# Kernel tuning notes

Measured on AMD Instinct MI355X. Metric: run time of the kernel, lower is better.

## Reference

```python
import jax, jax.numpy as jnp
import numpy as np

B, N, D = 8, 1024, 512
H, F = 8, 2048
Dh = D // H
EPS = 1e-5
NEG = -1.0e9


def _layernorm(x, g, b):
    mu = jnp.mean(x, axis=-1, keepdims=True)
    var = jnp.mean(jnp.square(x - mu), axis=-1, keepdims=True)
    return (x - mu) * jax.lax.rsqrt(var + EPS) * g + b


def setup_inputs() -> dict:
    key = jax.random.key(0)
    ks = jax.random.split(key, 8)
    s = 0.02  # weight init scale
    return {
        "x": jax.random.normal(ks[0], (B, N, D), jnp.float32),
        "adjacency_logits": jax.random.normal(ks[1], (N, N), jnp.float32),
        "candidate_edge_mask": jax.random.randint(ks[2], (N, N), 0, 2).astype(jnp.bool_),
        "Wq": jax.random.normal(ks[3], (D, D), jnp.float32) * s,
        "Wk": jax.random.normal(ks[4], (D, D), jnp.float32) * s,
        "Wv": jax.random.normal(ks[5], (D, D), jnp.float32) * s,
        "Wo": jax.random.normal(ks[6], (D, D), jnp.float32) * s,
        "W1": jax.random.normal(jax.random.fold_in(key, 10), (F, D), jnp.float32) * s,
        "b1": jnp.zeros((F,), jnp.float32),
        "W2": jax.random.normal(jax.random.fold_in(key, 11), (D, F), jnp.float32) * s,
        "b2": jnp.zeros((D,), jnp.float32),
        "g_ln1": jnp.ones((D,), jnp.float32),
        "beta_ln1": jnp.zeros((D,), jnp.float32),
        "g_ln2": jnp.ones((D,), jnp.float32),
        "beta_ln2": jnp.zeros((D,), jnp.float32),
    }


def reference(x, adjacency_logits, candidate_edge_mask, Wq, Wk, Wv, Wo,
              W1, b1, W2, b2, g_ln1, beta_ln1, g_ln2, beta_ln2):
    b, n, d = x.shape
    # projections: torch Linear is x @ W^T  -> [B,H,N,Dh]
    def proj(W):
        return jnp.einsum('bnd,ed->bne', x, W).reshape(b, n, H, Dh).transpose(0, 2, 1, 3)
    q, k, v = proj(Wq), proj(Wk), proj(Wv)
    scale = 1.0 / jnp.sqrt(jnp.float32(Dh))
    scores = jnp.einsum('bhqd,bhkd->bhqk', q, k) * scale
    scores = scores + adjacency_logits[None, None]
    mask = candidate_edge_mask[None, None]  # [1,1,N,N]
    scores = jnp.where(mask, scores, NEG)
    attn = jax.nn.softmax(scores, axis=-1)
    attn = jnp.where(mask, attn, 0.0)
    ctx = jnp.einsum('bhqk,bhkd->bhqd', attn, v)
    ctx = ctx.transpose(0, 2, 1, 3).reshape(b, n, d)
    attn_out = jnp.einsum('bnd,ed->bne', ctx, Wo)
    z = _layernorm(x + attn_out, g_ln1, beta_ln1)
    h = jax.nn.relu(jnp.einsum('bnd,fd->bnf', z, W1) + b1)
    z_ffn = jnp.einsum('bnf,df->bnd', h, W2) + b2
    out = _layernorm(z + z_ffn, g_ln2, beta_ln2)
    return out, attn.mean(axis=1)
```

## Files before the change

kernel.cpp:

```cpp
#include <hip/hip_runtime.h>
#include <math.h>
#include <stdint.h>


using bf16_t = __bf16;
typedef __attribute__((__ext_vector_type__(8))) __bf16 bf16x8;
typedef __attribute__((__ext_vector_type__(4))) __bf16 bf16x4;
typedef __attribute__((__ext_vector_type__(4))) float  f32x4;

#define DEVI __device__ __forceinline__

DEVI f32x4 mfma16(bf16x8 a, bf16x8 b, f32x4 c) {
  return __builtin_amdgcn_mfma_f32_16x16x32_bf16(a, b, c, 0, 0, 0);
}

DEVI void gload_lds16(const void* g, void* l) {
  __builtin_amdgcn_global_load_lds(
      (const __attribute__((address_space(1))) uint32_t*)g,
      (__attribute__((address_space(3))) uint32_t*)l, 16, 0, 0);
}

#define EPSC  (1e-5f)
#define QSCALE 0.18033688f

__global__ __launch_bounds__(256) void k_cvtall(const float* __restrict__ x,
                                                const float* __restrict__ wq,
                                                const float* __restrict__ wk,
                                                const float* __restrict__ wv,
                                                const float* __restrict__ wo,
                                                const float* __restrict__ w1,
                                                const float* __restrict__ w2,
                                                const float* __restrict__ adj,
                                                const int* __restrict__ msk,
                                                bf16_t* __restrict__ ox,
                                                bf16_t* __restrict__ owq,
                                                bf16_t* __restrict__ owk,
                                                bf16_t* __restrict__ owv,
                                                bf16_t* __restrict__ owo,
                                                bf16_t* __restrict__ ow1,
                                                bf16_t* __restrict__ ow2,
                                                bf16_t* __restrict__ eadjT) {
  int blk = blockIdx.x;
  if (blk >= 7168) {
    int row  = (blk - 7168) * 4 + (threadIdx.x >> 6);
    int lane = threadIdx.x & 63;
    for (int i = 0; i < 16; i++) {
      int c = lane + 64 * i;
      size_t idx = (size_t)row * 1024 + c;
      float a = adj[idx];
      bool valid = (msk[idx] != 0);
      int pos = (c & ~63) + (((c >> 2) & 3) << 4) + (((c >> 4) & 3) << 2) + (c & 3);
      eadjT[(size_t)row * 1024 + pos] = valid ? (__bf16)__expf(a) : (__bf16)0.f;
    }
    return;
  }
  const float* src; bf16_t* dst; int base;
  if (blk < 4096)      { src = x;  dst = ox;  base = blk; }
  else {
    blk -= 4096;
    if      (blk < 256)  { src = wq; dst = owq; base = blk; }
    else if (blk < 512)  { src = wk; dst = owk; base = blk - 256; }
    else if (blk < 768)  { src = wv; dst = owv; base = blk - 512; }
    else if (blk < 1024) { src = wo; dst = owo; base = blk - 768; }
    else if (blk < 2048) { src = w1; dst = ow1; base = blk - 1024; }
    else                 { src = w2; dst = ow2; base = blk - 2048; }
  }
  int i = base * 256 + threadIdx.x;
  float4 v = ((const float4*)src)[i];
  bf16x4 o = { (__bf16)v.x, (__bf16)v.y, (__bf16)v.z, (__bf16)v.w };
  ((bf16x4*)dst)[i] = o;
}

template<int EPI, int NSPLIT>
__global__ __launch_bounds__(256) void k_gemm(const bf16_t* __restrict__ A,
                                              const bf16_t* __restrict__ B,
                                              int K, int nbx,
                                              const float* __restrict__ bias,
                                              bf16_t* __restrict__ outb,
                                              int out_ncols) {
  __shared__ bf16_t lA[2][4096];
  __shared__ bf16_t lB[2][4096];
  int bid = blockIdx.x;
  int bps = 64 * nbx;
  int split = bid / bps, r = bid - split * bps;
  int nb = r % nbx, mb = r / nbx;
  int KS = K / NSPLIT;
  const bf16_t* Ab = A + (size_t)split * KS;
  const bf16_t* Bb = B + (size_t)split * KS;
  int tid = threadIdx.x, wid = tid >> 6, lane = tid & 63;
  int l16 = lane & 15, g = lane >> 4;
  int wr = wid >> 1, wc = wid & 1;
  int rowbase = mb * 128, c0 = nb * 128;

  int dA0 = wid * 2048 + lane * 16;
  int rA0 = dA0 >> 6;
  int cbA = ((dA0 >> 4) & 3) ^ (rA0 & 3);
  const bf16_t* Asrc0 = Ab + (size_t)(rowbase + rA0) * K + cbA * 8;
  const bf16_t* Asrc1 = Ab + (size_t)(rowbase + rA0 + 16) * K + cbA * 8;
  const bf16_t* Bsrc0 = Bb + (size_t)(c0 + rA0) * K + cbA * 8;
  const bf16_t* Bsrc1 = Bb + (size_t)(c0 + rA0 + 16) * K + cbA * 8;

  f32x4 acc[4][4];
#pragma unroll
  for (int m = 0; m < 4; m++)
#pragma unroll
    for (int n = 0; n < 4; n++) acc[m][n] = (f32x4){0.f, 0.f, 0.f, 0.f};

  gload_lds16(Asrc0, (char*)&lA[0][0] + wid * 2048);
  gload_lds16(Asrc1, (char*)&lA[0][0] + wid * 2048 + 1024);
  gload_lds16(Bsrc0, (char*)&lB[0][0] + wid * 2048);
  gload_lds16(Bsrc1, (char*)&lB[0][0] + wid * 2048 + 1024);
  __syncthreads();

  for (int k0 = 0; k0 < KS; k0 += 32) {
    int buf = (k0 >> 5) & 1;
    if (k0 + 32 < KS) {
      gload_lds16(Asrc0 + k0 + 32, (char*)&lA[buf ^ 1][0] + wid * 2048);
      gload_lds16(Asrc1 + k0 + 32, (char*)&lA[buf ^ 1][0] + wid * 2048 + 1024);
      gload_lds16(Bsrc0 + k0 + 32, (char*)&lB[buf ^ 1][0] + wid * 2048);
      gload_lds16(Bsrc1 + k0 + 32, (char*)&lB[buf ^ 1][0] + wid * 2048 + 1024);
    }
    const char* cA = (const char*)&lA[buf][0];
    const char* cB = (const char*)&lB[buf][0];
    bf16x8 af[4], bq[4];
#pragma unroll
    for (int m = 0; m < 4; m++) {
      int row = wr * 64 + m * 16 + l16;
      af[m] = *(const bf16x8*)(cA + row * 64 + ((g ^ (row & 3)) << 4));
    }
#pragma unroll
    for (int n = 0; n < 4; n++) {
      int row = wc * 64 + n * 16 + l16;
      bq[n] = *(const bf16x8*)(cB + row * 64 + ((g ^ (row & 3)) << 4));
    }
#pragma unroll
    for (int m = 0; m < 4; m++)
#pragma unroll
      for (int n = 0; n < 4; n++) acc[m][n] = mfma16(af[m], bq[n], acc[m][n]);
    __syncthreads();
  }

  int which = c0 / out_ncols;
  int cloc0 = c0 - which * out_ncols;
  size_t obase = (size_t)which * 8192 * out_ncols +
                 (size_t)split * 8192 * out_ncols * (NSPLIT > 1 ? 1 : 0);
  float osc = (EPI == 0 && which == 0) ? QSCALE : 1.0f;
#pragma unroll
  for (int n = 0; n < 4; n++) {
    int col = cloc0 + wc * 64 + n * 16 + l16;
    float bv = (EPI >= 1 && bias && split == 0) ? bias[col] : 0.f;
#pragma unroll
    for (int m = 0; m < 4; m++)
#pragma unroll
      for (int j = 0; j < 4; j++) {
        int row = rowbase + wr * 64 + m * 16 + g * 4 + j;
        float v = acc[m][n][j] + bv;
        size_t idx = obase + (size_t)row * out_ncols + col;
        if (EPI == 1) outb[idx] = (__bf16)fmaxf(v, 0.f);
        else if (EPI == 0) outb[idx] = (__bf16)(v * osc);
        else outb[idx] = (__bf16)v;
      }
  }
}

__global__ __launch_bounds__(256) void k_resln(const bf16_t* __restrict__ gin,
                                               int nsplit,
                                               const float* __restrict__ residf,
                                               const bf16_t* __restrict__ residb,
                                               const float* __restrict__ gam,
                                               const float* __restrict__ bet,
                                               float* __restrict__ outf,
                                               bf16_t* __restrict__ outb) {
  const size_t GS = (size_t)8192 * 512;
  int row = blockIdx.x * 4 + (threadIdx.x >> 6);
  int lane = threadIdx.x & 63;
  const bf16_t* gp = gin + (size_t)row * 512;
  float a[8];
  {
    bf16x8 v = ((const bf16x8*)gp)[lane];
#pragma unroll
    for (int e = 0; e < 8; e++) a[e] = (float)v[e];
  }
  for (int s = 1; s < nsplit; s++) {
    bf16x8 v = ((const bf16x8*)(gp + s * GS))[lane];
#pragma unroll
    for (int e = 0; e < 8; e++) a[e] += (float)v[e];
  }
  if (residf) {
    const float* rp = residf + (size_t)row * 512;
    float4 r0 = ((const float4*)rp)[2 * lane];
    float4 r1 = ((const float4*)rp)[2 * lane + 1];
    a[0] += r0.x; a[1] += r0.y; a[2] += r0.z; a[3] += r0.w;
    a[4] += r1.x; a[5] += r1.y; a[6] += r1.z; a[7] += r1.w;
  } else {
    bf16x8 r = ((const bf16x8*)(residb + (size_t)row * 512))[lane];
#pragma unroll
    for (int e = 0; e < 8; e++) a[e] += (float)r[e];
  }
  float s = 0.f;
#pragma unroll
  for (int e = 0; e < 8; e++) s += a[e];
  for (int off = 1; off < 64; off <<= 1) s += __shfl_xor(s, off);
  float mu = s * (1.f / 512.f);
  float sq = 0.f;
#pragma unroll
  for (int e = 0; e < 8; e++) { float d = a[e] - mu; sq += d * d; }
  for (int off = 1; off < 64; off <<= 1) sq += __shfl_xor(sq, off);
  float rs = rsqrtf(sq * (1.f / 512.f) + EPSC);

  float4 g0 = ((const float4*)gam)[2 * lane], g1v = ((const float4*)gam)[2 * lane + 1];
  float4 b0 = ((const float4*)bet)[2 * lane], b1v = ((const float4*)bet)[2 * lane + 1];
  float o[8];
  o[0] = (a[0] - mu) * rs * g0.x + b0.x;  o[1] = (a[1] - mu) * rs * g0.y + b0.y;
  o[2] = (a[2] - mu) * rs * g0.z + b0.z;  o[3] = (a[3] - mu) * rs * g0.w + b0.w;
  o[4] = (a[4] - mu) * rs * g1v.x + b1v.x; o[5] = (a[5] - mu) * rs * g1v.y + b1v.y;
  o[6] = (a[6] - mu) * rs * g1v.z + b1v.z; o[7] = (a[7] - mu) * rs * g1v.w + b1v.w;
  if (outf) {
    float* op = outf + (size_t)row * 512;
    ((float4*)op)[2 * lane]     = (float4){o[0], o[1], o[2], o[3]};
    ((float4*)op)[2 * lane + 1] = (float4){o[4], o[5], o[6], o[7]};
  }
  if (outb) {
    bf16x8 q;
#pragma unroll
    for (int e = 0; e < 8; e++) q[e] = (__bf16)o[e];
    ((bf16x8*)(outb + (size_t)row * 512))[lane] = q;
  }
}

__global__ __launch_bounds__(256) void k_vtrans_knorm(const bf16_t* __restrict__ v,
                                                      bf16_t* __restrict__ vT,
                                                      const bf16_t* __restrict__ kk,
                                                      float* __restrict__ kmax) {
  __shared__ bf16_t t[64 * 66];
  __shared__ float red[4];
  int bid = blockIdx.x;
  int tid = threadIdx.x, wid = tid >> 6, lane = tid & 63;
  if (bid < 1024) {
    int nt = bid & 15, h = (bid >> 4) & 7, b = bid >> 7;
    for (int i = 0; i < 16; i++) {
      int n = wid * 16 + i;
      t[lane * 66 + n] = v[(size_t)(b * 1024 + nt * 64 + n) * 512 + h * 64 + lane];
    }
    __syncthreads();
    int pi = (lane & 32) + (((lane >> 2) & 3) << 3) + (((lane >> 4) & 1) << 2) + (lane & 3);
    for (int i = 0; i < 16; i++) {
      int d = wid * 16 + i;
      vT[(size_t)((b * 8 + h) * 64 + d) * 1024 + nt * 64 + pi] = t[d * 66 + lane];
    }
  } else {
    int bh = bid - 1024;
    int b = bh >> 3, h = bh & 7;
    float mx = 0.f;
    for (int n = tid; n < 1024; n += 256) {
      const bf16_t* kp = kk + (size_t)(b * 1024 + n) * 512 + h * 64;
      float ss = 0.f;
#pragma unroll
      for (int vv = 0; vv < 8; vv++) {
        bf16x8 kv = *(const bf16x8*)(kp + vv * 8);
#pragma unroll
        for (int e = 0; e < 8; e++) { float f = (float)kv[e]; ss += f * f; }
      }
      mx = fmaxf(mx, ss);
    }
    for (int off = 1; off < 64; off <<= 1) mx = fmaxf(mx, __shfl_xor(mx, off));
    if (lane == 0) red[wid] = mx;
    __syncthreads();
    if (tid == 0) kmax[bh] = sqrtf(fmaxf(fmaxf(red[0], red[1]), fmaxf(red[2], red[3])));
  }
}

__global__ __launch_bounds__(512) void k_attn_ctx(const bf16_t* __restrict__ q,
                                                  const bf16_t* __restrict__ kk,
                                                  const bf16_t* __restrict__ vT,
                                                  const bf16_t* __restrict__ eadjT,
                                                  const float* __restrict__ kmax,
                                                  bf16_t* __restrict__ ctx,
                                                  float* __restrict__ crl) {
  __shared__ bf16_t ldsK[2][4096];
  __shared__ bf16_t ldsV[2][4096];
  int bid = blockIdx.x;
  int qt = bid >> 6, h = bid & 7, b = (bid >> 3) & 7;
  int tid = threadIdx.x, wid = tid >> 6, lane = tid & 63;
  int l16 = lane & 15, g = lane >> 4;
  int qg0 = qt * 128 + wid * 16;
  int kvbase = (b * 8 + h) * 64;

  int d0 = wid * 1024 + lane * 16;
  int row0 = d0 >> 7;
  int cb0 = ((d0 >> 4) & 7) ^ (row0 & 7);
  const bf16_t* ksrc = kk + (size_t)(b * 1024) * 512 + h * 64;
  const bf16_t* vsrc = vT + (size_t)kvbase * 1024;

  auto stage = [&](int buf, int kc0) {
    gload_lds16(ksrc + (size_t)(kc0 + row0) * 512 + cb0 * 8, &ldsK[buf][wid * 512]);
    gload_lds16(vsrc + (size_t)row0 * 1024 + kc0 + cb0 * 8, &ldsV[buf][wid * 512]);
  };

  const bf16_t* qp = q + (size_t)(b * 1024 + qg0 + l16) * 512 + h * 64 + 8 * g;
  bf16x8 aq0 = *(const bf16x8*)qp;
  bf16x8 aq1 = *(const bf16x8*)(qp + 32);

  float kmaxv = kmax[b * 8 + h];
  float ssq = 0.f;
#pragma unroll
  for (int e = 0; e < 8; e++) {
    float f0 = (float)aq0[e], f1 = (float)aq1[e];
    ssq += f0 * f0 + f1 * f1;
  }
  ssq += __shfl_xor(ssq, 16);
  ssq += __shfl_xor(ssq, 32);
  float Cn = sqrtf(ssq) * kmaxv;
  f32x4 negC4 = (f32x4){-Cn, -Cn, -Cn, -Cn};
  float Cj[4];
#pragma unroll
  for (int j = 0; j < 4; j++) Cj[j] = __shfl(Cn, g * 4 + j);

  bf16x8 ones;
#pragma unroll
  for (int e = 0; e < 8; e++) ones[e] = (__bf16)1.0f;

  f32x4 cacc[4];
#pragma unroll
  for (int d = 0; d < 4; d++) cacc[d] = (f32x4){0.f, 0.f, 0.f, 0.f};
  f32x4 lsacc = (f32x4){0.f, 0.f, 0.f, 0.f};
  int rph = l16 & 7;
  const bf16_t* erowT = eadjT + (size_t)(qg0 + l16) * 1024 + g * 16;

  bf16x8 eaA[2], eaB[2];
  auto loadEA = [&](bf16x8 (&d)[2], int kc0) {
    d[0] = *(const bf16x8*)(erowT + kc0);
    d[1] = *(const bf16x8*)(erowT + kc0 + 8);
  };

  auto cbar = [&]() {
    __builtin_amdgcn_sched_barrier(0);
    asm volatile("s_waitcnt vmcnt(2) lgkmcnt(0)" ::: "memory");
    __builtin_amdgcn_sched_barrier(0);
    __builtin_amdgcn_s_barrier();
    __builtin_amdgcn_sched_barrier(0);
  };

  auto tile = [&](int kt, int buf, bf16x8 (&eaC)[2], bf16x8 (&eaN)[2]) {
    int ktn = (kt + 1 < 16) ? kt + 1 : 15;
    stage(buf ^ 1, ktn * 64);
    loadEA(eaN, ktn * 64);

    const char* curK = (const char*)ldsK[buf];
    const char* curV = (const char*)ldsV[buf];

    bf16x8 pa0, pa1;
#pragma unroll
    for (int cg = 0; cg < 4; cg++) {
      const char* krow = curK + ((cg * 16 + l16) << 7);
      bf16x8 k0 = *(const bf16x8*)(krow + ((g ^ rph) << 4));
      bf16x8 k1 = *(const bf16x8*)(krow + (((g + 4) ^ rph) << 4));
      __builtin_amdgcn_s_setprio(1);
      f32x4 s = mfma16(k0, aq0, negC4);
      s = mfma16(k1, aq1, s);
      __builtin_amdgcn_s_setprio(0);
#pragma unroll
      for (int j = 0; j < 4; j++) {
        float p = (float)eaC[cg >> 1][(cg & 1) * 4 + j] * exp2f(s[j]);
        if (cg < 2) pa0[cg * 4 + j] = (__bf16)p;
        else        pa1[(cg - 2) * 4 + j] = (__bf16)p;
      }
    }
#pragma unroll
    for (int half = 0; half < 2; half++) {
      bf16x8 pa = half ? pa1 : pa0;
      __builtin_amdgcn_s_setprio(1);
#pragma unroll
      for (int dg = 0; dg < 4; dg++) {
        const char* vrow = curV + ((dg * 16 + l16) << 7);
        bf16x8 vv = *(const bf16x8*)(vrow + (((g + half * 4) ^ rph) << 4));
        cacc[dg] = mfma16(pa, vv, cacc[dg]);
      }
      lsacc = mfma16(pa, ones, lsacc);
      __builtin_amdgcn_s_setprio(0);
    }
    cbar();
  };

  stage(0, 0);
  loadEA(eaA, 0);
  cbar();

  for (int k2 = 0; k2 < 8; k2++) {
    tile(2 * k2,     0, eaA, eaB);
    tile(2 * k2 + 1, 1, eaB, eaA);
  }

  float rcj[4];
#pragma unroll
  for (int j = 0; j < 4; j++) rcj[j] = (lsacc[j] > 0.f) ? (1.f / lsacc[j]) : 0.f;

#pragma unroll
  for (int dg = 0; dg < 4; dg++)
#pragma unroll
    for (int j = 0; j < 4; j++) {
      int row = qg0 + g * 4 + j;
      ctx[(size_t)(b * 1024 + row) * 512 + h * 64 + dg * 16 + l16] =
          (__bf16)(cacc[dg][j] * rcj[j]);
    }
  if (l16 == 0) {
#pragma unroll
    for (int j = 0; j < 4; j++) {
      int li = (b * 8 + h) * 1024 + qg0 + g * 4 + j;
      crl[li] = (lsacc[j] > 0.f) ? (Cj[j] + __log2f(lsacc[j])) : 1.0e30f;
    }
  }
}

__global__ __launch_bounds__(256, 4) void k_attn_mean(const bf16_t* __restrict__ q,
                                                      const bf16_t* __restrict__ kk,
                                                      const bf16_t* __restrict__ eadjT,
                                                      const float* __restrict__ crl,
                                                      float* __restrict__ mout) {
  __shared__ bf16_t lds[4][2][2048];
  int bid = blockIdx.x;
  int kq = bid & 7, qt = (bid >> 3) & 15, b = bid >> 7;
  int tid = threadIdx.x, wid = tid >> 6, lane = tid & 63;
  int l16 = lane & 15, g = lane >> 4;
  int qg0 = qt * 64 + wid * 16;
  int kbase = kq * 128;
  int rl = lane >> 3;
  int cb = (lane & 7) ^ rl;
  const bf16_t* ksrc = kk + (size_t)(b * 1024 + kbase) * 512;

  auto stage = [&](int t) {
    int h = t >> 2, c = t & 3;
    char* dst = (char*)&lds[wid][t & 1][0];
    const bf16_t* sp = ksrc + (size_t)(c * 32 + rl) * 512 + h * 64 + cb * 8;
#pragma unroll
    for (int i = 0; i < 4; i++)
      gload_lds16(sp + (size_t)i * 8 * 512, dst + i * 1024);
  };

  f32x4 macc[8];
#pragma unroll
  for (int kg = 0; kg < 8; kg++) macc[kg] = (f32x4){0.f, 0.f, 0.f, 0.f};

  stage(0);

  for (int h = 0; h < 8; h++) {
    const bf16_t* qp = q + (size_t)(b * 1024 + qg0 + l16) * 512 + h * 64 + 8 * g;
    bf16x8 aq0 = *(const bf16x8*)qp;
    bf16x8 aq1 = *(const bf16x8*)(qp + 32);
    float CRs = crl[(b * 8 + h) * 1024 + qg0 + l16];
    f32x4 negCR4 = (f32x4){-CRs, -CRs, -CRs, -CRs};
#pragma unroll
    for (int c = 0; c < 4; c++) {
      int t = h * 4 + c;
      __builtin_amdgcn_sched_barrier(0);
      if (t < 31) {
        stage(t + 1);
        __builtin_amdgcn_sched_barrier(0);
        asm volatile("s_waitcnt vmcnt(4)" ::: "memory");
      } else {
        asm volatile("s_waitcnt vmcnt(0)" ::: "memory");
      }
      __builtin_amdgcn_sched_barrier(0);
      const char* cK = (const char*)&lds[wid][t & 1][0];
#pragma unroll
      for (int cg = 0; cg < 2; cg++) {
        const char* krow = cK + ((cg * 16 + l16) << 7);
        bf16x8 k0 = *(const bf16x8*)(krow + ((g ^ (l16 & 7)) << 4));
        bf16x8 k1 = *(const bf16x8*)(krow + (((g + 4) ^ (l16 & 7)) << 4));
        __builtin_amdgcn_s_setprio(1);
        f32x4 s = mfma16(k0, aq0, negCR4);
        s = mfma16(k1, aq1, s);
        __builtin_amdgcn_s_setprio(0);
        int kg = c * 2 + cg;
#pragma unroll
        for (int j = 0; j < 4; j++)
          macc[kg][j] += exp2f(s[j]);
      }
    }
  }

  const bf16_t* erowT = eadjT + (size_t)(qg0 + l16) * 1024 + kbase + g * 16;
  bf16x8 eA0 = *(const bf16x8*)(erowT);
  bf16x8 eA1 = *(const bf16x8*)(erowT + 8);
  bf16x8 eB0 = *(const bf16x8*)(erowT + 64);
  bf16x8 eB1 = *(const bf16x8*)(erowT + 72);
  float* mrow = mout + (size_t)b * 1048576 + (size_t)(qg0 + l16) * 1024 + kbase;
#pragma unroll
  for (int kg = 0; kg < 8; kg++) {
    bf16x8 eg = (kg < 2) ? eA0 : (kg < 4) ? eA1 : (kg < 6) ? eB0 : eB1;
    f32x4 mv;
#pragma unroll
    for (int j = 0; j < 4; j++)
      mv[j] = macc[kg][j] * (float)eg[(kg & 1) * 4 + j] * 0.125f;
    *(f32x4*)(mrow + kg * 16 + g * 4) = mv;
  }
}

extern "C" void kernel_launch(void* const* d_in, const int* in_sizes, int n_in,
                              void* d_out, int out_size, void* d_ws, size_t ws_size,
                              hipStream_t stream) {
  (void)in_sizes; (void)n_in; (void)out_size; (void)ws_size;
  const float* x   = (const float*)d_in[0];
  const float* adj = (const float*)d_in[1];
  const int*   msk = (const int*)d_in[2];
  const float* Wq  = (const float*)d_in[3];
  const float* Wk  = (const float*)d_in[4];
  const float* Wv  = (const float*)d_in[5];
  const float* Wo  = (const float*)d_in[6];
  const float* W1  = (const float*)d_in[7];
  const float* b1  = (const float*)d_in[8];
  const float* W2  = (const float*)d_in[9];
  const float* b2  = (const float*)d_in[10];
  const float* g1  = (const float*)d_in[11];
  const float* be1 = (const float*)d_in[12];
  const float* g2  = (const float*)d_in[13];
  const float* be2 = (const float*)d_in[14];

  float* out  = (float*)d_out;
  float* mout = out + (size_t)8 * 1024 * 512;

  char* ws = (char*)d_ws;
  const size_t MB = 1024 * 1024;
  bf16_t* wqb = (bf16_t*)(ws);
  bf16_t* wkb = (bf16_t*)(ws + 512 * 1024);
  bf16_t* wvb = (bf16_t*)(ws + 1 * MB);
  bf16_t* wob = (bf16_t*)(ws + 3 * MB / 2);
  bf16_t* w1b = (bf16_t*)(ws + 2 * MB);
  bf16_t* w2b = (bf16_t*)(ws + 4 * MB);
  float*  crl  = (float*)(ws + 6 * MB + 256 * 1024);
  float*  kmax = (float*)(ws + 6 * MB + 768 * 1024);
  bf16_t* xb   = (bf16_t*)(ws + 8 * MB);
  bf16_t* ctx  = xb;
  bf16_t* zb   = xb;
  bf16_t* qb   = (bf16_t*)(ws + 16 * MB);
  bf16_t* kb   = (bf16_t*)(ws + 24 * MB);
  bf16_t* vb   = (bf16_t*)(ws + 32 * MB);
  bf16_t* vT   = (bf16_t*)(ws + 40 * MB);
  bf16_t* gout1 = (bf16_t*)(ws + 16 * MB);
  bf16_t* hb    = (bf16_t*)(ws + 16 * MB);
  bf16_t* gout2 = (bf16_t*)(ws + 48 * MB);
  bf16_t* eadjT = (bf16_t*)(ws + 72 * MB);

  k_cvtall<<<7424, 256, 0, stream>>>(x, Wq, Wk, Wv, Wo, W1, W2, adj, msk,
                                     xb, wqb, wkb, wvb, wob, w1b, w2b, eadjT);

  k_gemm<0, 1><<<64 * 12, 256, 0, stream>>>(xb, wqb, 512, 12, nullptr, qb, 512);
  k_vtrans_knorm<<<1088, 256, 0, stream>>>(vb, vT, kb, kmax);

  k_attn_ctx<<<512, 512, 0, stream>>>(qb, kb, vT, eadjT, kmax, ctx, crl);
  k_attn_mean<<<1024, 256, 0, stream>>>(qb, kb, eadjT, crl, mout);

  k_gemm<2, 2><<<2 * 64 * 4, 256, 0, stream>>>(ctx, wob, 512, 4, nullptr, gout1, 512);
  k_resln<<<2048, 256, 0, stream>>>(gout1, 2, x, nullptr, g1, be1, nullptr, zb);
  k_gemm<1, 1><<<64 * 16, 256, 0, stream>>>(zb, w1b, 512, 16, b1, hb, 2048);
  k_gemm<2, 2><<<2 * 64 * 4, 256, 0, stream>>>(hb, w2b, 2048, 4, b2, gout2, 512);
  k_resln<<<2048, 256, 0, stream>>>(gout2, 2, nullptr, zb, g2, be2, out, nullptr);
}
```

Before: 212.3 us.

## Software-pipeline attention: overlap QK of tile k with PV of tile k-1

Splits the per-tile attention body into a QK/exp stage and a PV stage, then software-pipelines them so the current tile's QK MFMAs are issued alongside the previous tile's PV MFMAs. V gets a triple-buffered LDS ring so the previous tile's V stays resident while the next is staged. This aims to hide the exp/convert dependency latency between score computation and the PV matmul. In exchange it costs more LDS and keeps extra probability registers live, which may reduce occupancy.

```diff
diff --git a/kernel.cpp b/kernel.cpp
--- a/kernel.cpp
+++ b/kernel.cpp
@@ -278,7 +278,7 @@
                                                   bf16_t* __restrict__ ctx,
                                                   float* __restrict__ crl) {
   __shared__ bf16_t ldsK[2][4096];
-  __shared__ bf16_t ldsV[2][4096];
+  __shared__ bf16_t ldsV[3][4096];
   int bid = blockIdx.x;
   int qt = bid >> 6, h = bid & 7, b = (bid >> 3) & 7;
   int tid = threadIdx.x, wid = tid >> 6, lane = tid & 63;
@@ -292,8 +292,10 @@
   const bf16_t* ksrc = kk + (size_t)(b * 1024) * 512 + h * 64;
   const bf16_t* vsrc = vT + (size_t)kvbase * 1024;
 
-  auto stage = [&](int buf, int kc0) {
+  auto stageK = [&](int buf, int kc0) {
     gload_lds16(ksrc + (size_t)(kc0 + row0) * 512 + cb0 * 8, &ldsK[buf][wid * 512]);
+  };
+  auto stageV = [&](int buf, int kc0) {
     gload_lds16(vsrc + (size_t)row0 * 1024 + kc0 + cb0 * 8, &ldsV[buf][wid * 512]);
   };
 
@@ -341,15 +343,8 @@
     __builtin_amdgcn_sched_barrier(0);
   };
 
-  auto tile = [&](int kt, int buf, bf16x8 (&eaC)[2], bf16x8 (&eaN)[2]) {
-    int ktn = (kt + 1 < 16) ? kt + 1 : 15;
-    stage(buf ^ 1, ktn * 64);
-    loadEA(eaN, ktn * 64);
-
-    const char* curK = (const char*)ldsK[buf];
-    const char* curV = (const char*)ldsV[buf];
-
-    bf16x8 pa0, pa1;
+  auto qkTile = [&](int bufK, bf16x8 (&eaC)[2], bf16x8& pw0, bf16x8& pw1) {
+    const char* curK = (const char*)ldsK[bufK];
 #pragma unroll
     for (int cg = 0; cg < 4; cg++) {
       const char* krow = curK + ((cg * 16 + l16) << 7);
@@ -362,34 +357,62 @@
 #pragma unroll
       for (int j = 0; j < 4; j++) {
         float p = (float)eaC[cg >> 1][(cg & 1) * 4 + j] * exp2f(s[j]);
-        if (cg < 2) pa0[cg * 4 + j] = (__bf16)p;
-        else        pa1[(cg - 2) * 4 + j] = (__bf16)p;
+        if (cg < 2) pw0[cg * 4 + j] = (__bf16)p;
+        else        pw1[(cg - 2) * 4 + j] = (__bf16)p;
       }
     }
+  };
+
+  auto pvTile = [&](int vbuf, bf16x8& pr0, bf16x8& pr1) {
+    const char* prevV = (const char*)ldsV[vbuf];
 #pragma unroll
     for (int half = 0; half < 2; half++) {
-      bf16x8 pa = half ? pa1 : pa0;
+      bf16x8 pa = half ? pr1 : pr0;
       __builtin_amdgcn_s_setprio(1);
 #pragma unroll
       for (int dg = 0; dg < 4; dg++) {
-        const char* vrow = curV + ((dg * 16 + l16) << 7);
+        const char* vrow = prevV + ((dg * 16 + l16) << 7);
         bf16x8 vv = *(const bf16x8*)(vrow + (((g + half * 4) ^ rph) << 4));
         cacc[dg] = mfma16(pa, vv, cacc[dg]);
       }
       lsacc = mfma16(pa, ones, lsacc);
       __builtin_amdgcn_s_setprio(0);
     }
-    cbar();
-  };
-
-  stage(0, 0);
+  };
+
+  stageK(0, 0);
+  stageV(0, 0);
   loadEA(eaA, 0);
   cbar();
 
+  bf16x8 paA0, paA1, paB0, paB1;
+  int vP = 2, vC = 0, vN = 1;
+
   for (int k2 = 0; k2 < 8; k2++) {
-    tile(2 * k2,     0, eaA, eaB);
-    tile(2 * k2 + 1, 1, eaB, eaA);
-  }
+    {
+      int kt = 2 * k2;
+      int ktn = kt + 1;
+      stageK((kt & 1) ^ 1, ktn * 64);
+      stageV(vN, ktn * 64);
+      loadEA(eaB, ktn * 64);
+      qkTile(kt & 1, eaA, paA0, paA1);
+      if (k2 > 0) pvTile(vP, paB0, paB1);
+      cbar();
+      int t = vP; vP = vC; vC = vN; vN = t;
+    }
+    {
+      int kt = 2 * k2 + 1;
+      int ktn = (kt + 1 < 16) ? kt + 1 : 15;
+      stageK((kt & 1) ^ 1, ktn * 64);
+      stageV(vN, ktn * 64);
+      loadEA(eaA, ktn * 64);
+      qkTile(kt & 1, eaB, paB0, paB1);
+      pvTile(vP, paA0, paA1);
+      cbar();
+      int t = vP; vP = vC; vC = vN; vN = t;
+    }
+  }
+  pvTile(vP, paB0, paB1);
 
   float rcj[4];
 #pragma unroll
```

After: 212.4 us. Within noise of the previous version (+0.0%).
